# Optimization experiments

Hardware: AMD Instinct MI355X
Metric: run time of the kernel (lower is better)

## Reference

```python
import jax, jax.numpy as jnp
import numpy as np
from jax import lax

NUM_HEADS = 8
HEAD_SIZE = 256  # hidden_size // num_heads

def _layernorm(x, g, b, eps=1e-5):
    mu = jnp.mean(x, axis=-1, keepdims=True)
    var = jnp.mean((x - mu) ** 2, axis=-1, keepdims=True)
    return (x - mu) * lax.rsqrt(var + eps) * g + b

def _groupnorm(x, g, b, num_groups, eps=1e-5):
    B, C = x.shape
    xr = x.reshape(B, num_groups, C // num_groups)
    mu = jnp.mean(xr, axis=-1, keepdims=True)
    var = jnp.mean((xr - mu) ** 2, axis=-1, keepdims=True)
    xn = ((xr - mu) * lax.rsqrt(var + eps)).reshape(B, C)
    return xn * g + b

def _block_diag(x, W, b):
    # x: (B, nb*fi), W: (nb, fi, fo), b: (nb, fo) -> (B, nb*fo)
    B = x.shape[0]
    nb, fi, fo = W.shape
    y = jnp.einsum('bnf,nfo->bno', x.reshape(B, nb, fi), W) + b
    return y.reshape(B, nb * fo)

def _causal_conv1d(x, w, b):
    # x: (B, L); w: (1,1,4). Pad-both-sides-3 then drop last 3 == left-pad 3.
    y = lax.conv_general_dilated(x[:, None, :], w, (1,), [(3, 0)])
    return y[:, 0, :] + b

def _mlstm_forward(x, ln_g, ln_b, Wupl, bupl, Wupr, bupr, conv_w, conv_b,
                   Wskip, bskip, Wq, bq, Wk, bk, Wv, bv, Wi, bi, Wf, bf,
                   Wo, bo, gn_g, gn_b, Wdown, bdown, c_prev, n_prev, m_prev):
    x_norm = _layernorm(x, ln_g, ln_b)
    x_up_left = x_norm @ Wupl + bupl           # (B, 2D)
    x_up_right = x_norm @ Wupr + bupr          # (B, H)
    x_conv = jax.nn.silu(_causal_conv1d(x_up_left, conv_w, conv_b))
    x_skip = x_conv @ Wskip + bskip            # (B, H)
    q = _block_diag(x_conv, Wq, bq)
    k = _block_diag(x_conv, Wk, bk) / (HEAD_SIZE ** 0.5)
    v = _block_diag(x_up_left, Wv, bv)
    i_tilde = x_conv @ Wi + bi
    f_tilde = x_conv @ Wf + bf
    o = jax.nn.sigmoid(x_up_left @ Wo + bo)
    m_t = jnp.maximum(f_tilde + m_prev, i_tilde)
    i_g = jnp.exp(i_tilde - m_t)
    f_g = jnp.exp(f_tilde + m_prev - m_t)
    c_t = f_g * c_prev + i_g * (v * k)
    n_t = f_g * n_prev + i_g * k
    denom = jnp.max(jnp.abs(n_t.T @ q), axis=1)  # (H,) broadcast over batch
    h_t = o * (c_t * q) / denom
    out = _groupnorm(h_t, gn_g, gn_b, NUM_HEADS) + x_skip
    out = out * jax.nn.silu(x_up_right)
    final = out @ Wdown + bdown + x
    return (final, h_t, c_t, n_t, m_t)

def setup_inputs():
    key = jax.random.key(0)
    ks = jax.random.split(key, 16)
    B, D, H, NB = 8192, 1024, 2048, 8
    UP = 2 * D
    rnd = lambda k, shp, s=0.02: jax.random.normal(k, shp, jnp.float32) * s
    return {
        'x': jax.random.normal(ks[0], (B, D), jnp.float32),
        'ln_g': jnp.ones((D,), jnp.float32), 'ln_b': jnp.zeros((D,), jnp.float32),
        'Wupl': rnd(ks[1], (D, UP)), 'bupl': jnp.zeros((UP,), jnp.float32),
        'Wupr': rnd(ks[2], (D, H)), 'bupr': jnp.zeros((H,), jnp.float32),
        'conv_w': rnd(ks[3], (1, 1, 4), 0.3), 'conv_b': jnp.zeros((1,), jnp.float32),
        'Wskip': rnd(ks[4], (UP, H)), 'bskip': jnp.zeros((H,), jnp.float32),
        'Wq': rnd(ks[5], (NB, UP // NB, H // NB)), 'bq': jnp.zeros((NB, H // NB), jnp.float32),
        'Wk': rnd(ks[6], (NB, UP // NB, H // NB)), 'bk': jnp.zeros((NB, H // NB), jnp.float32),
        'Wv': rnd(ks[7], (NB, UP // NB, H // NB)), 'bv': jnp.zeros((NB, H // NB), jnp.float32),
        'Wi': rnd(ks[8], (UP, H)), 'bi': jnp.zeros((H,), jnp.float32),
        'Wf': rnd(ks[9], (UP, H)), 'bf': jnp.zeros((H,), jnp.float32),
        'Wo': rnd(ks[10], (UP, H)), 'bo': jnp.zeros((H,), jnp.float32),
        'gn_g': jnp.ones((H,), jnp.float32), 'gn_b': jnp.zeros((H,), jnp.float32),
        'Wdown': rnd(ks[11], (H, D)), 'bdown': jnp.zeros((D,), jnp.float32),
        'c_prev': rnd(ks[12], (B, H)), 'n_prev': jnp.ones((B, H), jnp.float32),
        'm_prev': jnp.zeros((B, H), jnp.float32),
    }

def reference(x, ln_g, ln_b, Wupl, bupl, Wupr, bupr, conv_w, conv_b, Wskip, bskip,
              Wq, bq, Wk, bk, Wv, bv, Wi, bi, Wf, bf, Wo, bo, gn_g, gn_b,
              Wdown, bdown, c_prev, n_prev, m_prev):
    return _mlstm_forward(x, ln_g, ln_b, Wupl, bupl, Wupr, bupr, conv_w, conv_b,
                          Wskip, bskip, Wq, bq, Wk, bk, Wv, bv, Wi, bi, Wf, bf,
                          Wo, bo, gn_g, gn_b, Wdown, bdown, c_prev, n_prev, m_prev)
```

## Files before the change

### kernel.cpp

```cpp
#include <hip/hip_runtime.h>


typedef __bf16 bf16_t;
typedef bf16_t bf16x8 __attribute__((ext_vector_type(8)));
typedef bf16_t bf16x4 __attribute__((ext_vector_type(4)));
typedef float f32x4 __attribute__((ext_vector_type(4)));

#define B_ROWS 8192
#define DMODEL 1024
#define HDIM   2048

__device__ __forceinline__ void gload_lds16(const void* g, void* s) {
  __builtin_amdgcn_global_load_lds(
      (const __attribute__((address_space(1))) void*)g,
      (__attribute__((address_space(3))) void*)s, 16, 0, 0);
}

__device__ __forceinline__ float sigmoidf_(float x) { return 1.f / (1.f + __expf(-x)); }
__device__ __forceinline__ float siluf_(float x)    { return x / (1.f + __expf(-x)); }

__global__ __launch_bounds__(256) void wtrans_kernel(
    const float* __restrict__ in, bf16_t* __restrict__ out, int R, int C) {
  const int z = blockIdx.z;
  in  += (size_t)z * R * C;
  out += (size_t)z * R * C;
  __shared__ float tile[64][65];
  const int t = threadIdx.x;
  const int r0 = blockIdx.y * 64, c0 = blockIdx.x * 64;
#pragma unroll
  for (int j = 0; j < 4; ++j) {
    const int r = j * 16 + (t >> 4);
    const int c = (t & 15) * 4;
    float4 v = *(const float4*)&in[(size_t)(r0 + r) * C + c0 + c];
    tile[r][c] = v.x; tile[r][c + 1] = v.y; tile[r][c + 2] = v.z; tile[r][c + 3] = v.w;
  }
  __syncthreads();
#pragma unroll
  for (int j = 0; j < 2; ++j) {
    const int wi = j * 256 + t;
    const int oc = wi >> 3;
    const int orr = (wi & 7) * 8;
    bf16x8 v;
#pragma unroll
    for (int u = 0; u < 8; ++u) v[u] = (bf16_t)tile[orr + u][oc];
    *(bf16x8*)&out[(size_t)(c0 + oc) * R + r0 + orr] = v;
  }
}

__global__ __launch_bounds__(256) void ln_kernel(
    const float* __restrict__ x, const float* __restrict__ g,
    const float* __restrict__ b, bf16_t* __restrict__ out) {
  const int row = blockIdx.x;
  const int t = threadIdx.x;
  const float* xr = x + (size_t)row * DMODEL;
  float4 v = *(const float4*)&xr[t * 4];
  float s = v.x + v.y + v.z + v.w;
  float s2 = v.x * v.x + v.y * v.y + v.z * v.z + v.w * v.w;
#pragma unroll
  for (int off = 1; off < 64; off <<= 1) {
    s += __shfl_xor(s, off, 64);
    s2 += __shfl_xor(s2, off, 64);
  }
  __shared__ float ps[8];
  const int w = t >> 6;
  if ((t & 63) == 0) { ps[w] = s; ps[4 + w] = s2; }
  __syncthreads();
  s = ps[0] + ps[1] + ps[2] + ps[3];
  s2 = ps[4] + ps[5] + ps[6] + ps[7];
  const float mu = s / (float)DMODEL;
  const float var = s2 / (float)DMODEL - mu * mu;
  const float rstd = rsqrtf(var + 1e-5f);
  float4 gg = *(const float4*)&g[t * 4];
  float4 bb = *(const float4*)&b[t * 4];
  bf16x4 o;
  o[0] = (bf16_t)((v.x - mu) * rstd * gg.x + bb.x);
  o[1] = (bf16_t)((v.y - mu) * rstd * gg.y + bb.y);
  o[2] = (bf16_t)((v.z - mu) * rstd * gg.z + bb.z);
  o[3] = (bf16_t)((v.w - mu) * rstd * gg.w + bb.w);
  *(bf16x4*)&out[(size_t)row * DMODEL + t * 4] = o;
}

__global__ __launch_bounds__(256) void conv_kernel(
    const bf16_t* __restrict__ xin, const float* __restrict__ cw,
    const float* __restrict__ cb, bf16_t* __restrict__ yb) {
  const size_t idx = (size_t)blockIdx.x * blockDim.x + threadIdx.x;
  const int row = (int)(idx >> 9);
  const int c0 = ((int)idx & 511) * 4;
  const bf16_t* xr = xin + (size_t)row * HDIM;
  const float w0 = cw[0], w1 = cw[1], w2 = cw[2], w3 = cw[3], bb = cb[0];
  float xm3 = 0.f, xm2 = 0.f, xm1 = 0.f;
  if (c0 > 0) {
    bf16x4 p = *(const bf16x4*)&xr[c0 - 4];
    xm3 = (float)p[1]; xm2 = (float)p[2]; xm1 = (float)p[3];
  }
  bf16x4 xv4 = *(const bf16x4*)&xr[c0];
  float x0 = (float)xv4[0], x1 = (float)xv4[1], x2 = (float)xv4[2], x3 = (float)xv4[3];
  float y0 = w0 * xm3 + w1 * xm2 + w2 * xm1 + w3 * x0 + bb;
  float y1 = w0 * xm2 + w1 * xm1 + w2 * x0 + w3 * x1 + bb;
  float y2 = w0 * xm1 + w1 * x0 + w2 * x1 + w3 * x2 + bb;
  float y3 = w0 * x0 + w1 * x1 + w2 * x2 + w3 * x3 + bb;
  bf16x4 yb4;
  yb4[0] = (bf16_t)siluf_(y0); yb4[1] = (bf16_t)siluf_(y1);
  yb4[2] = (bf16_t)siluf_(y2); yb4[3] = (bf16_t)siluf_(y3);
  *(bf16x4*)&yb[(size_t)row * HDIM + c0] = yb4;
}

__global__ __launch_bounds__(256) void hgn_kernel(
    const bf16_t* __restrict__ o_pre, const float* __restrict__ q,
    const float* __restrict__ c_t, const float* __restrict__ denomf,
    const bf16_t* __restrict__ skip, const bf16_t* __restrict__ upr,
    const float* __restrict__ gn_g, const float* __restrict__ gn_b,
    float* __restrict__ h_out, bf16_t* __restrict__ act_out) {
  const int row = blockIdx.x;
  const int t = threadIdx.x;
  const size_t base = (size_t)row * HDIM + t * 8;
  const int i0 = t * 8;
  bf16x8 o8 = *(const bf16x8*)&o_pre[base];
  float h[8];
  float s = 0.f, s2 = 0.f;
#pragma unroll
  for (int j = 0; j < 2; ++j) {
    float4 qv = *(const float4*)&q[base + j * 4];
    float4 cv = *(const float4*)&c_t[base + j * 4];
#pragma unroll
    for (int u = 0; u < 4; ++u) {
      const int k = j * 4 + u;
      float hv = sigmoidf_((float)o8[k]) * ((const float*)&cv)[u] *
                 ((const float*)&qv)[u] / denomf[i0 + k];
      h[k] = hv;
      s += hv;
      s2 += hv * hv;
    }
  }
#pragma unroll
  for (int off = 1; off < 32; off <<= 1) {
    s += __shfl_xor(s, off, 64);
    s2 += __shfl_xor(s2, off, 64);
  }
  const float mu = s / 256.f;
  const float var = s2 / 256.f - mu * mu;
  const float rstd = rsqrtf(var + 1e-5f);
  float4 h0 = {h[0], h[1], h[2], h[3]};
  float4 h1 = {h[4], h[5], h[6], h[7]};
  *(float4*)&h_out[base] = h0;
  *(float4*)&h_out[base + 4] = h1;
  bf16x8 sk8 = *(const bf16x8*)&skip[base];
  bf16x8 up8 = *(const bf16x8*)&upr[base];
  bf16x8 a8;
#pragma unroll
  for (int j = 0; j < 2; ++j) {
    float4 gv = *(const float4*)&gn_g[i0 + j * 4];
    float4 bv = *(const float4*)&gn_b[i0 + j * 4];
#pragma unroll
    for (int u = 0; u < 4; ++u) {
      const int k = j * 4 + u;
      float y = (h[k] - mu) * rstd * ((const float*)&gv)[u] + ((const float*)&bv)[u];
      y = (y + (float)sk8[k]) * siluf_((float)up8[k]);
      a8[k] = (bf16_t)y;
    }
  }
  *(bf16x8*)&act_out[base] = a8;
}

template <int OUTMODE, bool RES>
__global__ __launch_bounds__(256) void gemm_kernel(
    const bf16_t* __restrict__ A, int lda, const bf16_t* __restrict__ Bt, int ldb,
    const float* __restrict__ bias, float* __restrict__ C, bf16_t* __restrict__ Cb,
    int ldc, const float* __restrict__ res, int ldres, int K, float scale,
    int zA, long long zB, int zBias, int zC) {
  const int z = blockIdx.z;
  A += (size_t)z * zA;
  Bt += (size_t)z * zB;
  if (bias) bias += (size_t)z * zBias;
  if (OUTMODE == 0) C += (size_t)z * zC; else Cb += (size_t)z * zC;
  const int brow = blockIdx.y * 128;
  const int bcol = blockIdx.x * 128;
  __shared__ bf16_t As[128 * 32];
  __shared__ bf16_t Bs[128 * 32];
  const int tid = threadIdx.x;
  const int w = tid >> 6, l = tid & 63;
  const int wr = w >> 1, wc = w & 1;
  const int lr = l & 15, kg = l >> 4;
  const int l4 = l & 3, ld4 = l >> 2;

  f32x4 acc[4][4];
  const f32x4 fzero = {0.f, 0.f, 0.f, 0.f};
#pragma unroll
  for (int m = 0; m < 4; ++m)
#pragma unroll
    for (int n = 0; n < 4; ++n) acc[m][n] = fzero;

  for (int kt = 0; kt < K; kt += 32) {
#pragma unroll
    for (int j = 0; j < 2; ++j) {
      const int rowX = w * 32 + j * 16 + ld4;
      gload_lds16(A + (size_t)(brow + rowX) * lda + kt + l4 * 8, &As[w * 1024 + j * 512]);
      gload_lds16(Bt + (size_t)(bcol + rowX) * ldb + kt + l4 * 8, &Bs[w * 1024 + j * 512]);
    }
    __syncthreads();
    bf16x8 a[4], b[4];
#pragma unroll
    for (int m = 0; m < 4; ++m)
      a[m] = *(const bf16x8*)&As[(wr * 64 + m * 16 + lr) * 32 + kg * 8];
#pragma unroll
    for (int n = 0; n < 4; ++n)
      b[n] = *(const bf16x8*)&Bs[(wc * 64 + n * 16 + lr) * 32 + kg * 8];
#pragma unroll
    for (int m = 0; m < 4; ++m)
#pragma unroll
      for (int n = 0; n < 4; ++n)
        acc[m][n] = __builtin_amdgcn_mfma_f32_16x16x32_bf16(a[m], b[n], acc[m][n], 0, 0, 0);
    __syncthreads();
  }

#pragma unroll
  for (int m = 0; m < 4; ++m) {
    const int row0 = brow + wr * 64 + m * 16 + kg * 4;
#pragma unroll
    for (int n = 0; n < 4; ++n) {
      const int col = bcol + wc * 64 + n * 16 + lr;
      const float bv = bias ? bias[col] : 0.f;
#pragma unroll
      for (int r = 0; r < 4; ++r) {
        const int row = row0 + r;
        float v = (acc[m][n][r] + bv) * scale;
        if (RES) v += res[(size_t)row * ldres + col];
        if (OUTMODE == 0) C[(size_t)row * ldc + col] = v;
        else Cb[(size_t)row * ldc + col] = (bf16_t)v;
      }
    }
  }
}

__global__ __launch_bounds__(256) void gemm_ifgate_kernel(
    const bf16_t* __restrict__ A,
    const bf16_t* __restrict__ Bi, const bf16_t* __restrict__ Bf,
    const float* __restrict__ bi, const float* __restrict__ bfv,
    const float* __restrict__ m_prev, const float* __restrict__ c_prev,
    const float* __restrict__ n_prev,
    const bf16_t* __restrict__ vb, const bf16_t* __restrict__ kb,
    float* __restrict__ m_out, float* __restrict__ c_out, float* __restrict__ n_out) {
  const int brow = blockIdx.y * 128;
  const int bcol = blockIdx.x * 64;
  __shared__ bf16_t As[128 * 32];
  __shared__ bf16_t Bis[64 * 32];
  __shared__ bf16_t Bfs[64 * 32];
  const int tid = threadIdx.x;
  const int w = tid >> 6, l = tid & 63;
  const int wr = w >> 1, wc = w & 1;
  const int lr = l & 15, kg = l >> 4;
  const int l4 = l & 3, ld4 = l >> 2;

  f32x4 acci[4][2], accf[4][2];
  const f32x4 fzero = {0.f, 0.f, 0.f, 0.f};
#pragma unroll
  for (int m = 0; m < 4; ++m)
#pragma unroll
    for (int n = 0; n < 2; ++n) { acci[m][n] = fzero; accf[m][n] = fzero; }

  for (int kt = 0; kt < HDIM; kt += 32) {
#pragma unroll
    for (int j = 0; j < 2; ++j) {
      const int rowX = w * 32 + j * 16 + ld4;
      gload_lds16(A + (size_t)(brow + rowX) * HDIM + kt + l4 * 8, &As[w * 1024 + j * 512]);
    }
    const int rowB = bcol + w * 16 + ld4;
    gload_lds16(Bi + (size_t)rowB * HDIM + kt + l4 * 8, &Bis[w * 512]);
    gload_lds16(Bf + (size_t)rowB * HDIM + kt + l4 * 8, &Bfs[w * 512]);
    __syncthreads();
    bf16x8 a[4], b1[2], b2[2];
#pragma unroll
    for (int m = 0; m < 4; ++m)
      a[m] = *(const bf16x8*)&As[(wr * 64 + m * 16 + lr) * 32 + kg * 8];
#pragma unroll
    for (int n = 0; n < 2; ++n) {
      b1[n] = *(const bf16x8*)&Bis[(wc * 32 + n * 16 + lr) * 32 + kg * 8];
      b2[n] = *(const bf16x8*)&Bfs[(wc * 32 + n * 16 + lr) * 32 + kg * 8];
    }
#pragma unroll
    for (int m = 0; m < 4; ++m)
#pragma unroll
      for (int n = 0; n < 2; ++n) {
        acci[m][n] = __builtin_amdgcn_mfma_f32_16x16x32_bf16(a[m], b1[n], acci[m][n], 0, 0, 0);
        accf[m][n] = __builtin_amdgcn_mfma_f32_16x16x32_bf16(a[m], b2[n], accf[m][n], 0, 0, 0);
      }
    __syncthreads();
  }

#pragma unroll
  for (int m = 0; m < 4; ++m) {
    const int row0 = brow + wr * 64 + m * 16 + kg * 4;
#pragma unroll
    for (int n = 0; n < 2; ++n) {
      const int col = bcol + wc * 32 + n * 16 + lr;
      const float biv = bi[col], bfvv = bfv[col];
#pragma unroll
      for (int r = 0; r < 4; ++r) {
        const int row = row0 + r;
        const size_t idx = (size_t)row * HDIM + col;
        const float it = acci[m][n][r] + biv;
        const float ft = accf[m][n][r] + bfvv;
        const float m1 = m_prev[idx];
        const float mt = fmaxf(ft + m1, it);
        const float ig = __expf(it - mt);
        const float fg = __expf(ft + m1 - mt);
        const float v1 = (float)vb[idx], k1 = (float)kb[idx];
        m_out[idx] = mt;
        c_out[idx] = fg * c_prev[idx] + ig * (v1 * k1);
        n_out[idx] = fg * n_prev[idx] + ig * k1;
      }
    }
  }
}

__global__ __launch_bounds__(256) void denom_reduce_kernel(
    const float* __restrict__ part, float* __restrict__ dmaxf) {
  const int i = blockIdx.x;
  const int t = threadIdx.x;
  float vmax = 0.f;
#pragma unroll
  for (int u = 0; u < 8; ++u) {
    const int j = u * 256 + t;
    float s = 0.f;
#pragma unroll
    for (int zz = 0; zz < 8; ++zz)
      s += part[(size_t)zz * HDIM * HDIM + (size_t)i * HDIM + j];
    vmax = fmaxf(vmax, fabsf(s));
  }
#pragma unroll
  for (int off = 1; off < 64; off <<= 1) vmax = fmaxf(vmax, __shfl_xor(vmax, off, 64));
  __shared__ float ps[4];
  if ((t & 63) == 0) ps[t >> 6] = vmax;
  __syncthreads();
  if (t == 0) dmaxf[i] = fmaxf(fmaxf(ps[0], ps[1]), fmaxf(ps[2], ps[3]));
}

extern "C" void kernel_launch(void* const* d_in, const int* in_sizes, int n_in,
                              void* d_out, int out_size, void* d_ws, size_t ws_size,
                              hipStream_t stream) {
  (void)in_sizes; (void)n_in; (void)out_size; (void)ws_size;
  const float* x      = (const float*)d_in[0];
  const float* ln_g   = (const float*)d_in[1];
  const float* ln_b   = (const float*)d_in[2];
  const float* Wupl   = (const float*)d_in[3];
  const float* bupl   = (const float*)d_in[4];
  const float* Wupr   = (const float*)d_in[5];
  const float* bupr   = (const float*)d_in[6];
  const float* conv_w = (const float*)d_in[7];
  const float* conv_b = (const float*)d_in[8];
  const float* Wskip  = (const float*)d_in[9];
  const float* bskip  = (const float*)d_in[10];
  const float* Wq     = (const float*)d_in[11];
  const float* bq     = (const float*)d_in[12];
  const float* Wk     = (const float*)d_in[13];
  const float* bk     = (const float*)d_in[14];
  const float* Wv     = (const float*)d_in[15];
  const float* bv     = (const float*)d_in[16];
  const float* Wi     = (const float*)d_in[17];
  const float* bi     = (const float*)d_in[18];
  const float* Wf     = (const float*)d_in[19];
  const float* bf_    = (const float*)d_in[20];
  const float* Wo     = (const float*)d_in[21];
  const float* bo     = (const float*)d_in[22];
  const float* gn_g   = (const float*)d_in[23];
  const float* gn_b   = (const float*)d_in[24];
  const float* Wdown  = (const float*)d_in[25];
  const float* bdown  = (const float*)d_in[26];
  const float* c_prev = (const float*)d_in[27];
  const float* n_prev = (const float*)d_in[28];
  const float* m_prev = (const float*)d_in[29];

  float* out_final = (float*)d_out;
  float* out_h = out_final + (size_t)B_ROWS * DMODEL;
  float* out_c = out_h + (size_t)B_ROWS * HDIM;
  float* out_n = out_c + (size_t)B_ROWS * HDIM;
  float* out_m = out_n + (size_t)B_ROWS * HDIM;

  char* ws = (char*)d_ws;
  size_t off = 0;
  auto alloc = [&](size_t bytes) -> void* {
    off = (off + 255) & ~(size_t)255;
    void* p = ws + off;
    off += bytes;
    return p;
  };
  const size_t BH = (size_t)B_ROWS * HDIM;
  const size_t BD = (size_t)B_ROWS * DMODEL;

  bf16_t* WuplT = (bf16_t*)alloc((size_t)DMODEL * HDIM * 2);
  bf16_t* WuprT = (bf16_t*)alloc((size_t)DMODEL * HDIM * 2);
  bf16_t* WskipT = (bf16_t*)alloc((size_t)HDIM * HDIM * 2);
  bf16_t* WiT = (bf16_t*)alloc((size_t)HDIM * HDIM * 2);
  bf16_t* WfT = (bf16_t*)alloc((size_t)HDIM * HDIM * 2);
  bf16_t* WoT = (bf16_t*)alloc((size_t)HDIM * HDIM * 2);
  bf16_t* WdownT = (bf16_t*)alloc((size_t)HDIM * DMODEL * 2);
  bf16_t* WqT = (bf16_t*)alloc((size_t)8 * 256 * 256 * 2);
  bf16_t* WkT = (bf16_t*)alloc((size_t)8 * 256 * 256 * 2);
  bf16_t* WvT = (bf16_t*)alloc((size_t)8 * 256 * 256 * 2);
  bf16_t* xnorm_b = (bf16_t*)alloc(BD * 2);
  bf16_t* xupl_b = (bf16_t*)alloc(BH * 2);
  bf16_t* xupr_b = (bf16_t*)alloc(BH * 2);
  bf16_t* xconv_b = (bf16_t*)alloc(BH * 2);
  bf16_t* xskip_b = (bf16_t*)alloc(BH * 2);
  bf16_t* o_b = (bf16_t*)alloc(BH * 2);
  float*  q_f = (float*)alloc(BH * 4);
  bf16_t* k_b = (bf16_t*)alloc(BH * 2);
  bf16_t* v_b = (bf16_t*)alloc(BH * 2);
  bf16_t* qT_b = (bf16_t*)alloc(BH * 2);
  bf16_t* nT_b = (bf16_t*)alloc(BH * 2);
  bf16_t* act_b = (bf16_t*)alloc(BH * 2);
  float*  part = (float*)alloc((size_t)8 * HDIM * HDIM * 4);
  float*  dmaxf = (float*)alloc(HDIM * 4);

  wtrans_kernel<<<dim3(HDIM / 64, DMODEL / 64, 1), 256, 0, stream>>>(Wupl, WuplT, DMODEL, HDIM);
  wtrans_kernel<<<dim3(HDIM / 64, DMODEL / 64, 1), 256, 0, stream>>>(Wupr, WuprT, DMODEL, HDIM);
  wtrans_kernel<<<dim3(HDIM / 64, HDIM / 64, 1), 256, 0, stream>>>(Wskip, WskipT, HDIM, HDIM);
  wtrans_kernel<<<dim3(HDIM / 64, HDIM / 64, 1), 256, 0, stream>>>(Wi, WiT, HDIM, HDIM);
  wtrans_kernel<<<dim3(HDIM / 64, HDIM / 64, 1), 256, 0, stream>>>(Wf, WfT, HDIM, HDIM);
  wtrans_kernel<<<dim3(HDIM / 64, HDIM / 64, 1), 256, 0, stream>>>(Wo, WoT, HDIM, HDIM);
  wtrans_kernel<<<dim3(DMODEL / 64, HDIM / 64, 1), 256, 0, stream>>>(Wdown, WdownT, HDIM, DMODEL);
  wtrans_kernel<<<dim3(4, 4, 8), 256, 0, stream>>>(Wq, WqT, 256, 256);
  wtrans_kernel<<<dim3(4, 4, 8), 256, 0, stream>>>(Wk, WkT, 256, 256);
  wtrans_kernel<<<dim3(4, 4, 8), 256, 0, stream>>>(Wv, WvT, 256, 256);

  ln_kernel<<<B_ROWS, 256, 0, stream>>>(x, ln_g, ln_b, xnorm_b);

  gemm_kernel<2, false><<<dim3(HDIM / 128, B_ROWS / 128, 1), 256, 0, stream>>>(
      xnorm_b, DMODEL, WuplT, DMODEL, bupl, nullptr, xupl_b, HDIM, nullptr, 0,
      DMODEL, 1.f, 0, 0, 0, 0);
  gemm_kernel<2, false><<<dim3(HDIM / 128, B_ROWS / 128, 1), 256, 0, stream>>>(
      xnorm_b, DMODEL, WuprT, DMODEL, bupr, nullptr, xupr_b, HDIM, nullptr, 0,
      DMODEL, 1.f, 0, 0, 0, 0);

  conv_kernel<<<(unsigned)(BH / 4 / 256), 256, 0, stream>>>(xupl_b, conv_w, conv_b, xconv_b);

  gemm_kernel<2, false><<<dim3(HDIM / 128, B_ROWS / 128, 1), 256, 0, stream>>>(
      xconv_b, HDIM, WskipT, HDIM, bskip, nullptr, xskip_b, HDIM, nullptr, 0,
      HDIM, 1.f, 0, 0, 0, 0);
  gemm_kernel<2, false><<<dim3(HDIM / 128, B_ROWS / 128, 1), 256, 0, stream>>>(
      xupl_b, HDIM, WoT, HDIM, bo, nullptr, o_b, HDIM, nullptr, 0,
      HDIM, 1.f, 0, 0, 0, 0);

  gemm_kernel<0, false><<<dim3(2, B_ROWS / 128, 8), 256, 0, stream>>>(
      xconv_b, HDIM, WqT, 256, bq, q_f, nullptr, HDIM, nullptr, 0,
      256, 1.f, 256, 256 * 256, 256, 256);
  gemm_kernel<2, false><<<dim3(2, B_ROWS / 128, 8), 256, 0, stream>>>(
      xconv_b, HDIM, WkT, 256, bk, nullptr, k_b, HDIM, nullptr, 0,
      256, 0.0625f, 256, 256 * 256, 256, 256);
  gemm_kernel<2, false><<<dim3(2, B_ROWS / 128, 8), 256, 0, stream>>>(
      xupl_b, HDIM, WvT, 256, bv, nullptr, v_b, HDIM, nullptr, 0,
      256, 1.f, 256, 256 * 256, 256, 256);

  gemm_ifgate_kernel<<<dim3(HDIM / 64, B_ROWS / 128, 1), 256, 0, stream>>>(
      xconv_b, WiT, WfT, bi, bf_, m_prev, c_prev, n_prev, v_b, k_b,
      out_m, out_c, out_n);

  wtrans_kernel<<<dim3(HDIM / 64, B_ROWS / 64, 1), 256, 0, stream>>>(q_f, qT_b, B_ROWS, HDIM);
  wtrans_kernel<<<dim3(HDIM / 64, B_ROWS / 64, 1), 256, 0, stream>>>(out_n, nT_b, B_ROWS, HDIM);

  gemm_kernel<0, false><<<dim3(HDIM / 128, HDIM / 128, 8), 256, 0, stream>>>(
      nT_b, B_ROWS, qT_b, B_ROWS, nullptr, part, nullptr, HDIM, nullptr, 0,
      1024, 1.f, 1024, 1024, 0, HDIM * HDIM);
  denom_reduce_kernel<<<HDIM, 256, 0, stream>>>(part, dmaxf);

  hgn_kernel<<<B_ROWS, 256, 0, stream>>>(o_b, q_f, out_c, dmaxf, xskip_b,
                                         xupr_b, gn_g, gn_b, out_h, act_b);

  gemm_kernel<0, true><<<dim3(DMODEL / 128, B_ROWS / 128, 1), 256, 0, stream>>>(
      act_b, HDIM, WdownT, HDIM, bdown, out_final, nullptr, DMODEL, x, DMODEL,
      HDIM, 1.f, 0, 0, 0, 0);
}
```

Baseline: 1.546 ms.

## Add 256x256 double-buffered swizzled GEMM kernel with XCD remapping for large GEMMs

Adds a new GEMM kernel with 512-thread blocks and 256x256 tiles. It uses a K-step of 64, double-buffered LDS staging through direct global-to-LDS loads, and XOR-swizzled LDS layouts to avoid bank conflicts. Workgroups are remapped across XCDs for cache locality, and MFMA sections run at raised priority. The i/f-gate fused GEMM gets the same treatment, and the split-K denominator GEMM drops from 8 to 4 partitions, which halves the partial buffer and the reduction work. Larger tiles raise register and LDS pressure and reduce the number of blocks for the smaller GEMMs, such as Wdown with only 128 blocks.

```diff
diff --git a/kernel.cpp b/kernel.cpp
--- a/kernel.cpp
+++ b/kernel.cpp
@@ -18,6 +18,12 @@
 
 __device__ __forceinline__ float sigmoidf_(float x) { return 1.f / (1.f + __expf(-x)); }
 __device__ __forceinline__ float siluf_(float x)    { return x / (1.f + __expf(-x)); }
+
+__device__ __forceinline__ int xcd_swz(int lin, int nwg) {
+  const int q = nwg >> 3, r = nwg & 7;
+  const int xcd = lin & 7, sub = lin >> 3;
+  return (xcd < r ? xcd * (q + 1) : r * (q + 1) + (xcd - r) * q) + sub;
+}
 
 __global__ __launch_bounds__(256) void wtrans_kernel(
     const float* __restrict__ in, bf16_t* __restrict__ out, int R, int C) {
@@ -232,7 +238,109 @@
   }
 }
 
-__global__ __launch_bounds__(256) void gemm_ifgate_kernel(
+template <int OUTMODE , bool RES>
+__global__ __launch_bounds__(512, 2) void gemm256_kernel(
+    const bf16_t* __restrict__ A, int lda, const bf16_t* __restrict__ Bt, int ldb,
+    const float* __restrict__ bias, float* __restrict__ C, bf16_t* __restrict__ Cb,
+    int ldc, const float* __restrict__ res, int ldres, int K, float scale,
+    long long zA, long long zB, long long zC) {
+  const int z = blockIdx.z;
+  A += (size_t)z * zA;
+  Bt += (size_t)z * zB;
+  if (OUTMODE == 0) C += (size_t)z * zC; else Cb += (size_t)z * zC;
+
+  const int nwg = gridDim.x * gridDim.y;
+  const int lin2 = xcd_swz(blockIdx.y * gridDim.x + blockIdx.x, nwg);
+  const int bx = lin2 % gridDim.x, by = lin2 / gridDim.x;
+  const int brow = by * 256, bcol = bx * 256;
+
+  __shared__ bf16_t As[2][256 * 64];
+  __shared__ bf16_t Bs[2][256 * 64];
+
+  const int tid = threadIdx.x;
+  const int l = tid & 63;
+  const int w = tid >> 6;
+  const int wr = w >> 2, wn = w & 3;
+  const int lr = l & 15, kg = l >> 4;
+  const int srow = tid >> 3;
+  const int sslot = (tid & 7) ^ (srow & 7);
+
+  f32x4 acc[8][4];
+  const f32x4 fzero = {0.f, 0.f, 0.f, 0.f};
+#pragma unroll
+  for (int m = 0; m < 8; ++m)
+#pragma unroll
+    for (int n = 0; n < 4; ++n) acc[m][n] = fzero;
+
+  const int NT = K >> 6;
+  const bf16_t* Ag = A + (size_t)brow * lda;
+  const bf16_t* Bg = Bt + (size_t)bcol * ldb;
+
+  auto stage = [&](int t, int buf) {
+    const size_t kof = (size_t)t * 64 + sslot * 8;
+#pragma unroll
+    for (int j = 0; j < 4; ++j) {
+      const int r = j * 64 + srow;
+      gload_lds16(Ag + (size_t)r * lda + kof, (char*)&As[buf][0] + (j * 512 + tid) * 16);
+      gload_lds16(Bg + (size_t)r * ldb + kof, (char*)&Bs[buf][0] + (j * 512 + tid) * 16);
+    }
+  };
+
+  stage(0, 0);
+  stage(1, 1);
+
+  for (int t = 0; t < NT; ++t) {
+    if (t < NT - 1) asm volatile("s_waitcnt vmcnt(8)" ::: "memory");
+    else            asm volatile("s_waitcnt vmcnt(0)" ::: "memory");
+    __builtin_amdgcn_s_barrier();
+    const int buf = t & 1;
+#pragma unroll
+    for (int kk = 0; kk < 2; ++kk) {
+      bf16x8 a[8], b[4];
+#pragma unroll
+      for (int n = 0; n < 4; ++n) {
+        const int r = wn * 64 + n * 16 + lr;
+        b[n] = *(const bf16x8*)&Bs[buf][r * 64 + (((kk * 4 + kg) ^ (r & 7)) * 8)];
+      }
+#pragma unroll
+      for (int m = 0; m < 8; ++m) {
+        const int r = wr * 128 + m * 16 + lr;
+        a[m] = *(const bf16x8*)&As[buf][r * 64 + (((kk * 4 + kg) ^ (r & 7)) * 8)];
+      }
+      __builtin_amdgcn_s_setprio(1);
+#pragma unroll
+      for (int m = 0; m < 8; ++m)
+#pragma unroll
+        for (int n = 0; n < 4; ++n)
+          acc[m][n] = __builtin_amdgcn_mfma_f32_16x16x32_bf16(a[m], b[n], acc[m][n], 0, 0, 0);
+      __builtin_amdgcn_s_setprio(0);
+    }
+    asm volatile("s_waitcnt lgkmcnt(0)" ::: "memory");
+    __builtin_amdgcn_sched_barrier(0);
+    __builtin_amdgcn_s_barrier();
+    if (t + 2 < NT) stage(t + 2, buf);
+  }
+
+#pragma unroll
+  for (int m = 0; m < 8; ++m) {
+    const int row0 = brow + wr * 128 + m * 16 + kg * 4;
+#pragma unroll
+    for (int n = 0; n < 4; ++n) {
+      const int col = bcol + wn * 64 + n * 16 + lr;
+      const float bvv = bias ? bias[col] : 0.f;
+#pragma unroll
+      for (int r = 0; r < 4; ++r) {
+        const int row = row0 + r;
+        float v = (acc[m][n][r] + bvv) * scale;
+        if (RES) v += res[(size_t)row * ldres + col];
+        if (OUTMODE == 0) C[(size_t)row * ldc + col] = v;
+        else Cb[(size_t)row * ldc + col] = (bf16_t)v;
+      }
+    }
+  }
+}
+
+__global__ __launch_bounds__(512, 2) void ifgate256_kernel(
     const bf16_t* __restrict__ A,
     const bf16_t* __restrict__ Bi, const bf16_t* __restrict__ Bf,
     const float* __restrict__ bi, const float* __restrict__ bfv,
@@ -240,59 +348,95 @@
     const float* __restrict__ n_prev,
     const bf16_t* __restrict__ vb, const bf16_t* __restrict__ kb,
     float* __restrict__ m_out, float* __restrict__ c_out, float* __restrict__ n_out) {
-  const int brow = blockIdx.y * 128;
-  const int bcol = blockIdx.x * 64;
-  __shared__ bf16_t As[128 * 32];
-  __shared__ bf16_t Bis[64 * 32];
-  __shared__ bf16_t Bfs[64 * 32];
+  const int nwg = gridDim.x * gridDim.y;
+  const int lin2 = xcd_swz(blockIdx.y * gridDim.x + blockIdx.x, nwg);
+  const int bx = lin2 % gridDim.x, by = lin2 / gridDim.x;
+  const int brow = by * 256, bcol = bx * 128;
+
+  __shared__ bf16_t As[2][256 * 64];
+  __shared__ bf16_t Bis[2][128 * 64];
+  __shared__ bf16_t Bfs[2][128 * 64];
+
   const int tid = threadIdx.x;
-  const int w = tid >> 6, l = tid & 63;
-  const int wr = w >> 1, wc = w & 1;
+  const int l = tid & 63;
+  const int w = tid >> 6;
+  const int wr = w >> 2, wn = w & 3;
   const int lr = l & 15, kg = l >> 4;
-  const int l4 = l & 3, ld4 = l >> 2;
-
-  f32x4 acci[4][2], accf[4][2];
+  const int srow = tid >> 3;
+  const int sslot = (tid & 7) ^ (srow & 7);
+
+  f32x4 acci[8][2], accf[8][2];
   const f32x4 fzero = {0.f, 0.f, 0.f, 0.f};
 #pragma unroll
-  for (int m = 0; m < 4; ++m)
+  for (int m = 0; m < 8; ++m)
 #pragma unroll
     for (int n = 0; n < 2; ++n) { acci[m][n] = fzero; accf[m][n] = fzero; }
 
-  for (int kt = 0; kt < HDIM; kt += 32) {
+  const int NT = HDIM >> 6;
+  const bf16_t* Ag = A + (size_t)brow * HDIM;
+  const bf16_t* Big = Bi + (size_t)bcol * HDIM;
+  const bf16_t* Bfg = Bf + (size_t)bcol * HDIM;
+
+  auto stage = [&](int t, int buf) {
+    const size_t kof = (size_t)t * 64 + sslot * 8;
+#pragma unroll
+    for (int j = 0; j < 4; ++j) {
+      const int r = j * 64 + srow;
+      gload_lds16(Ag + (size_t)r * HDIM + kof, (char*)&As[buf][0] + (j * 512 + tid) * 16);
+    }
 #pragma unroll
     for (int j = 0; j < 2; ++j) {
-      const int rowX = w * 32 + j * 16 + ld4;
-      gload_lds16(A + (size_t)(brow + rowX) * HDIM + kt + l4 * 8, &As[w * 1024 + j * 512]);
-    }
-    const int rowB = bcol + w * 16 + ld4;
-    gload_lds16(Bi + (size_t)rowB * HDIM + kt + l4 * 8, &Bis[w * 512]);
-    gload_lds16(Bf + (size_t)rowB * HDIM + kt + l4 * 8, &Bfs[w * 512]);
-    __syncthreads();
-    bf16x8 a[4], b1[2], b2[2];
-#pragma unroll
-    for (int m = 0; m < 4; ++m)
-      a[m] = *(const bf16x8*)&As[(wr * 64 + m * 16 + lr) * 32 + kg * 8];
+      const int r = j * 64 + srow;
+      gload_lds16(Big + (size_t)r * HDIM + kof, (char*)&Bis[buf][0] + (j * 512 + tid) * 16);
+      gload_lds16(Bfg + (size_t)r * HDIM + kof, (char*)&Bfs[buf][0] + (j * 512 + tid) * 16);
+    }
+  };
+
+  stage(0, 0);
+  stage(1, 1);
+
+  for (int t = 0; t < NT; ++t) {
+    if (t < NT - 1) asm volatile("s_waitcnt vmcnt(8)" ::: "memory");
+    else            asm volatile("s_waitcnt vmcnt(0)" ::: "memory");
+    __builtin_amdgcn_s_barrier();
+    const int buf = t & 1;
+#pragma unroll
+    for (int kk = 0; kk < 2; ++kk) {
+      bf16x8 a[8], b1[2], b2[2];
+#pragma unroll
+      for (int n = 0; n < 2; ++n) {
+        const int r = wn * 32 + n * 16 + lr;
+        const int eo = r * 64 + (((kk * 4 + kg) ^ (r & 7)) * 8);
+        b1[n] = *(const bf16x8*)&Bis[buf][eo];
+        b2[n] = *(const bf16x8*)&Bfs[buf][eo];
+      }
+#pragma unroll
+      for (int m = 0; m < 8; ++m) {
+        const int r = wr * 128 + m * 16 + lr;
+        a[m] = *(const bf16x8*)&As[buf][r * 64 + (((kk * 4 + kg) ^ (r & 7)) * 8)];
+      }
+      __builtin_amdgcn_s_setprio(1);
+#pragma unroll
+      for (int m = 0; m < 8; ++m)
+#pragma unroll
+        for (int n = 0; n < 2; ++n) {
+          acci[m][n] = __builtin_amdgcn_mfma_f32_16x16x32_bf16(a[m], b1[n], acci[m][n], 0, 0, 0);
+          accf[m][n] = __builtin_amdgcn_mfma_f32_16x16x32_bf16(a[m], b2[n], accf[m][n], 0, 0, 0);
+        }
+      __builtin_amdgcn_s_setprio(0);
+    }
+    asm volatile("s_waitcnt lgkmcnt(0)" ::: "memory");
+    __builtin_amdgcn_sched_barrier(0);
+    __builtin_amdgcn_s_barrier();
+    if (t + 2 < NT) stage(t + 2, buf);
+  }
+
+#pragma unroll
+  for (int m = 0; m < 8; ++m) {
+    const int row0 = brow + wr * 128 + m * 16 + kg * 4;
 #pragma unroll
     for (int n = 0; n < 2; ++n) {
-      b1[n] = *(const bf16x8*)&Bis[(wc * 32 + n * 16 + lr) * 32 + kg * 8];
-      b2[n] = *(const bf16x8*)&Bfs[(wc * 32 + n * 16 + lr) * 32 + kg * 8];
-    }
-#pragma unroll
-    for (int m = 0; m < 4; ++m)
-#pragma unroll
-      for (int n = 0; n < 2; ++n) {
-        acci[m][n] = __builtin_amdgcn_mfma_f32_16x16x32_bf16(a[m], b1[n], acci[m][n], 0, 0, 0);
-        accf[m][n] = __builtin_amdgcn_mfma_f32_16x16x32_bf16(a[m], b2[n], accf[m][n], 0, 0, 0);
-      }
-    __syncthreads();
-  }
-
-#pragma unroll
-  for (int m = 0; m < 4; ++m) {
-    const int row0 = brow + wr * 64 + m * 16 + kg * 4;
-#pragma unroll
-    for (int n = 0; n < 2; ++n) {
-      const int col = bcol + wc * 32 + n * 16 + lr;
+      const int col = bcol + wn * 32 + n * 16 + lr;
       const float biv = bi[col], bfvv = bfv[col];
 #pragma unroll
       for (int r = 0; r < 4; ++r) {
@@ -323,7 +467,7 @@
     const int j = u * 256 + t;
     float s = 0.f;
 #pragma unroll
-    for (int zz = 0; zz < 8; ++zz)
+    for (int zz = 0; zz < 4; ++zz)
       s += part[(size_t)zz * HDIM * HDIM + (size_t)i * HDIM + j];
     vmax = fmaxf(vmax, fabsf(s));
   }
@@ -409,7 +553,7 @@
   bf16_t* qT_b = (bf16_t*)alloc(BH * 2);
   bf16_t* nT_b = (bf16_t*)alloc(BH * 2);
   bf16_t* act_b = (bf16_t*)alloc(BH * 2);
-  float*  part = (float*)alloc((size_t)8 * HDIM * HDIM * 4);
+  float*  part = (float*)alloc((size_t)4 * HDIM * HDIM * 4);
   float*  dmaxf = (float*)alloc(HDIM * 4);
 
   wtrans_kernel<<<dim3(HDIM / 64, DMODEL / 64, 1), 256, 0, stream>>>(Wupl, WuplT, DMODEL, HDIM);
@@ -425,21 +569,21 @@
 
   ln_kernel<<<B_ROWS, 256, 0, stream>>>(x, ln_g, ln_b, xnorm_b);
 
-  gemm_kernel<2, false><<<dim3(HDIM / 128, B_ROWS / 128, 1), 256, 0, stream>>>(
+  gemm256_kernel<2, false><<<dim3(HDIM / 256, B_ROWS / 256, 1), 512, 0, stream>>>(
       xnorm_b, DMODEL, WuplT, DMODEL, bupl, nullptr, xupl_b, HDIM, nullptr, 0,
-      DMODEL, 1.f, 0, 0, 0, 0);
-  gemm_kernel<2, false><<<dim3(HDIM / 128, B_ROWS / 128, 1), 256, 0, stream>>>(
+      DMODEL, 1.f, 0, 0, 0);
+  gemm256_kernel<2, false><<<dim3(HDIM / 256, B_ROWS / 256, 1), 512, 0, stream>>>(
       xnorm_b, DMODEL, WuprT, DMODEL, bupr, nullptr, xupr_b, HDIM, nullptr, 0,
-      DMODEL, 1.f, 0, 0, 0, 0);
+      DMODEL, 1.f, 0, 0, 0);
 
   conv_kernel<<<(unsigned)(BH / 4 / 256), 256, 0, stream>>>(xupl_b, conv_w, conv_b, xconv_b);
 
-  gemm_kernel<2, false><<<dim3(HDIM / 128, B_ROWS / 128, 1), 256, 0, stream>>>(
+  gemm256_kernel<2, false><<<dim3(HDIM / 256, B_ROWS / 256, 1), 512, 0, stream>>>(
       xconv_b, HDIM, WskipT, HDIM, bskip, nullptr, xskip_b, HDIM, nullptr, 0,
-      HDIM, 1.f, 0, 0, 0, 0);
-  gemm_kernel<2, false><<<dim3(HDIM / 128, B_ROWS / 128, 1), 256, 0, stream>>>(
+      HDIM, 1.f, 0, 0, 0);
+  gemm256_kernel<2, false><<<dim3(HDIM / 256, B_ROWS / 256, 1), 512, 0, stream>>>(
       xupl_b, HDIM, WoT, HDIM, bo, nullptr, o_b, HDIM, nullptr, 0,
-      HDIM, 1.f, 0, 0, 0, 0);
+      HDIM, 1.f, 0, 0, 0);
 
   gemm_kernel<0, false><<<dim3(2, B_ROWS / 128, 8), 256, 0, stream>>>(
       xconv_b, HDIM, WqT, 256, bq, q_f, nullptr, HDIM, nullptr, 0,
@@ -451,22 +595,22 @@
       xupl_b, HDIM, WvT, 256, bv, nullptr, v_b, HDIM, nullptr, 0,
       256, 1.f, 256, 256 * 256, 256, 256);
 
-  gemm_ifgate_kernel<<<dim3(HDIM / 64, B_ROWS / 128, 1), 256, 0, stream>>>(
+  ifgate256_kernel<<<dim3(HDIM / 128, B_ROWS / 256, 1), 512, 0, stream>>>(
       xconv_b, WiT, WfT, bi, bf_, m_prev, c_prev, n_prev, v_b, k_b,
       out_m, out_c, out_n);
 
   wtrans_kernel<<<dim3(HDIM / 64, B_ROWS / 64, 1), 256, 0, stream>>>(q_f, qT_b, B_ROWS, HDIM);
   wtrans_kernel<<<dim3(HDIM / 64, B_ROWS / 64, 1), 256, 0, stream>>>(out_n, nT_b, B_ROWS, HDIM);
 
-  gemm_kernel<0, false><<<dim3(HDIM / 128, HDIM / 128, 8), 256, 0, stream>>>(
+  gemm256_kernel<0, false><<<dim3(HDIM / 256, HDIM / 256, 4), 512, 0, stream>>>(
       nT_b, B_ROWS, qT_b, B_ROWS, nullptr, part, nullptr, HDIM, nullptr, 0,
-      1024, 1.f, 1024, 1024, 0, HDIM * HDIM);
+      2048, 1.f, 2048, 2048, (long long)HDIM * HDIM);
   denom_reduce_kernel<<<HDIM, 256, 0, stream>>>(part, dmaxf);
 
   hgn_kernel<<<B_ROWS, 256, 0, stream>>>(o_b, q_f, out_c, dmaxf, xskip_b,
                                          xupr_b, gn_g, gn_b, out_h, act_b);
 
-  gemm_kernel<0, true><<<dim3(DMODEL / 128, B_ROWS / 128, 1), 256, 0, stream>>>(
+  gemm256_kernel<0, true><<<dim3(DMODEL / 256, B_ROWS / 256, 1), 512, 0, stream>>>(
       act_b, HDIM, WdownT, HDIM, bdown, out_final, nullptr, DMODEL, x, DMODEL,
-      HDIM, 1.f, 0, 0, 0, 0);
-}
+      HDIM, 1.f, 0, 0, 0);
+}
```

Result: faster. 1.351 ms (-12.6%).
